# Kernel optimization log

Hardware: AMD Instinct MI355X
Metric: run time of the kernel (lower is better)

Reference implementation:

```python
import jax, jax.numpy as jnp
import numpy as np

N_NODES = 50000
N_EDGES = 800000
N_GRAPHS = 64
IN_C = 256      # num_commodities
HID = 256       # hidden_units
HID2 = HID // 2
N_DCS = 64


def setup_inputs() -> dict:
    key = jax.random.key(0)
    ks = jax.random.split(key, 8)
    x = jax.random.normal(ks[0], (N_NODES, IN_C), dtype=jnp.float32)
    edge_index = jax.random.randint(ks[1], (2, N_EDGES), 0, N_NODES, dtype=jnp.int32)
    # sorted graph-membership ids; even partition guarantees no empty graph
    batch = ((jnp.arange(N_NODES) * N_GRAPHS) // N_NODES).astype(jnp.int32)
    s1 = 1.0 / np.sqrt(IN_C)
    s2 = 1.0 / np.sqrt(HID)
    s3 = 1.0 / np.sqrt(HID2)
    W1 = jax.random.normal(ks[2], (IN_C, HID), dtype=jnp.float32) * s1
    b1 = jnp.zeros((HID,), dtype=jnp.float32)
    W2 = jax.random.normal(ks[3], (HID, HID2), dtype=jnp.float32) * s2
    b2 = jnp.zeros((HID2,), dtype=jnp.float32)
    Wm = jax.random.normal(ks[4], (HID2, N_DCS), dtype=jnp.float32) * s3
    bm = jax.random.normal(ks[5], (N_DCS,), dtype=jnp.float32) * s3
    return {"x": x, "edge_index": edge_index, "batch": batch,
            "W1": W1, "b1": b1, "W2": W2, "b2": b2, "Wm": Wm, "bm": bm}


def gcn_conv(x, W, b, src, dst, n_nodes):
    """PyG GCNConv: D^{-1/2}(A+I)D^{-1/2} X W + b (self-loops added)."""
    h = x @ W                                    # [N, out]
    ones = jnp.ones(src.shape[0], dtype=h.dtype)
    deg = jax.ops.segment_sum(ones, dst, num_segments=n_nodes) + 1.0  # +1 self-loop
    dis = jax.lax.rsqrt(deg)                     # deg >= 1, safe
    norm = dis[src] * dis[dst]                   # [E]
    agg = jax.ops.segment_sum(h[src] * norm[:, None], dst, num_segments=n_nodes)
    agg = agg + h * (dis * dis)[:, None]         # self-loop contribution
    return agg + b


def reference(x, edge_index, batch, W1, b1, W2, b2, Wm, bm):
    src, dst = edge_index[0], edge_index[1]
    n = x.shape[0]
    bx = jax.nn.relu(gcn_conv(x, W1, b1, src, dst, n))
    cx = jax.nn.relu(gcn_conv(bx, W2, b2, src, dst, n))
    px = jax.ops.segment_max(cx, batch, num_segments=N_GRAPHS)  # global max pool
    return px @ Wm + bm                           # [N_GRAPHS, N_DCS]
```

## Files before the change

### kernel.cpp

```cpp
#include <hip/hip_runtime.h>
#include <cstdint>


typedef _Float16 half2v __attribute__((ext_vector_type(2)));
typedef _Float16 half4v __attribute__((ext_vector_type(4)));
typedef _Float16 half8v __attribute__((ext_vector_type(8)));
typedef float f32x4 __attribute__((ext_vector_type(4)));

__device__ __forceinline__ void gl_lds16(const void* g, void* l) {
  __builtin_amdgcn_global_load_lds(
      (const __attribute__((address_space(1))) unsigned int*)g,
      (__attribute__((address_space(3))) unsigned int*)l, 16, 0, 0);
}

__global__ void deg_cvtw_k(const int* __restrict__ dst, int* __restrict__ deg,
                           int E, int ndeg,
                           const float* __restrict__ W1, _Float16* __restrict__ Wt1,
                           const float* __restrict__ W2, _Float16* __restrict__ Wt2) {
  const int b = blockIdx.x;
  if (b >= ndeg) {
    int i = (b - ndeg) * 256 + threadIdx.x;
    if (i < 256 * 256) {
      int k = i >> 8, c = i & 255;
      Wt1[c * 256 + k] = (_Float16)W1[i];
    } else {
      int j = i - 256 * 256;
      if (j < 256 * 128) {
        int k = j >> 7, c = j & 127;
        Wt2[c * 256 + k] = (_Float16)W2[j];
      }
    }
    return;
  }
  int i = b * blockDim.x + threadIdx.x;
  int e0 = i * 4;
  if (e0 + 4 <= E) {
    int4 d = *(const int4*)(dst + e0);
    atomicAdd(&deg[d.x], 1);
    atomicAdd(&deg[d.y], 1);
    atomicAdd(&deg[d.z], 1);
    atomicAdd(&deg[d.w], 1);
  } else {
    for (int e = e0; e < E; ++e) atomicAdd(&deg[dst[e]], 1);
  }
}

__global__ __launch_bounds__(256) void prep_k(const int* __restrict__ deg,
                                              int* __restrict__ offs,
                                              float* __restrict__ dis, int n) {
  __shared__ int sd[256];
  const int b = blockIdx.x;
  int pre = 0;
  for (int j = threadIdx.x; j < b * 256; j += 256) pre += deg[j];
  sd[threadIdx.x] = pre;
  __syncthreads();
  for (int s = 128; s > 0; s >>= 1) {
    if (threadIdx.x < s) sd[threadIdx.x] += sd[threadIdx.x + s];
    __syncthreads();
  }
  const int boff = sd[0];
  __syncthreads();
  int i = b * 256 + threadIdx.x;
  int v = (i < n) ? deg[i] : 0;
  if (i < n) dis[i] = rsqrtf((float)v + 1.0f);
  sd[threadIdx.x] = v;
  __syncthreads();
  for (int d = 1; d < 256; d <<= 1) {
    int t = (threadIdx.x >= d) ? sd[threadIdx.x - d] : 0;
    __syncthreads();
    sd[threadIdx.x] += t;
    __syncthreads();
  }
  if (i < n) offs[i] = boff + sd[threadIdx.x] - v;
  if (i == n - 1) offs[n] = boff + sd[threadIdx.x];
}

__global__ __launch_bounds__(256) void fill_gemm1_k(
    const int* __restrict__ src, const int* __restrict__ dstv,
    const int* __restrict__ offs, int* __restrict__ deg,
    unsigned short* __restrict__ csr, int E, int nfill,
    const float* __restrict__ A, const _Float16* __restrict__ Bt,
    const float* __restrict__ dis, _Float16* __restrict__ C, int M) {
  constexpr int K = 256, N = 256, BM = 64, BK = 32;
  __shared__ _Float16 As[BM * BK];
  __shared__ _Float16 Bs[N * BK];

  if (blockIdx.x < nfill) {
    int i = blockIdx.x * blockDim.x + threadIdx.x;
    int e0 = i * 4;
    if (e0 + 4 <= E) {
      int4 d = *(const int4*)(dstv + e0);
      int4 s = *(const int4*)(src + e0);
      int p0 = atomicSub(&deg[d.x], 1) - 1;
      csr[offs[d.x] + p0] = (unsigned short)s.x;
      int p1 = atomicSub(&deg[d.y], 1) - 1;
      csr[offs[d.y] + p1] = (unsigned short)s.y;
      int p2 = atomicSub(&deg[d.z], 1) - 1;
      csr[offs[d.z] + p2] = (unsigned short)s.z;
      int p3 = atomicSub(&deg[d.w], 1) - 1;
      csr[offs[d.w] + p3] = (unsigned short)s.w;
    } else {
      for (int e = e0; e < E; ++e) {
        int d = dstv[e];
        int pos = atomicSub(&deg[d], 1) - 1;
        csr[offs[d] + pos] = (unsigned short)src[e];
      }
    }
    return;
  }

  const int tid = threadIdx.x, lane = tid & 63, wave = tid >> 6;
  const int row0 = (blockIdx.x - nfill) * BM;
  const int kbase = (lane >> 4) * 8;
  const int r16 = lane & 15;

  int arow = row0 + wave * 16 + r16;
  if (arow > M - 1) arow = M - 1;
  const float* aSrc = A + (size_t)arow * K + kbase;
  _Float16* aDst = As + wave * 512 + lane * 8;

  const _Float16* bSrc[4];
  _Float16* bDst[4];
#pragma unroll
  for (int hh = 0; hh < 4; ++hh) {
    int fl = hh * 4 + wave;
    bSrc[hh] = Bt + (size_t)(fl * 16 + r16) * K + kbase;
    bDst[hh] = Bs + fl * 512;
  }

  f32x4 acc[4][4] = {};
  for (int k0 = 0; k0 < K; k0 += BK) {
#pragma unroll
    for (int hh = 0; hh < 4; ++hh) gl_lds16(bSrc[hh] + k0, bDst[hh]);
    float4 a0 = *(const float4*)(aSrc + k0);
    float4 a1 = *(const float4*)(aSrc + k0 + 4);
    half8v ah = {(_Float16)a0.x, (_Float16)a0.y, (_Float16)a0.z, (_Float16)a0.w,
                 (_Float16)a1.x, (_Float16)a1.y, (_Float16)a1.z, (_Float16)a1.w};
    *(half8v*)aDst = ah;
    __syncthreads();

    half8v af[4], bf[4];
#pragma unroll
    for (int m = 0; m < 4; ++m)
      af[m] = *(const half8v*)(As + m * 512 + lane * 8);
#pragma unroll
    for (int nj = 0; nj < 4; ++nj)
      bf[nj] = *(const half8v*)(Bs + (wave * 4 + nj) * 512 + lane * 8);
#pragma unroll
    for (int m = 0; m < 4; ++m)
#pragma unroll
      for (int nj = 0; nj < 4; ++nj)
        acc[m][nj] = __builtin_amdgcn_mfma_f32_16x16x32_f16(af[m], bf[nj], acc[m][nj], 0, 0, 0);
    __syncthreads();
  }

#pragma unroll
  for (int m = 0; m < 4; ++m) {
    const int rbase = row0 + m * 16 + (lane >> 4) * 4;
    float dr[4];
#pragma unroll
    for (int r = 0; r < 4; ++r) dr[r] = (rbase + r < M) ? dis[rbase + r] : 0.f;
#pragma unroll
    for (int nj = 0; nj < 4; ++nj) {
      int col = wave * 64 + nj * 16 + r16;
#pragma unroll
      for (int r = 0; r < 4; ++r) {
        int row = rbase + r;
        if (row < M) C[(size_t)row * N + col] = (_Float16)(acc[m][nj][r] * dr[r]);
      }
    }
  }
}

#define GBM 128
#define GBN 128
#define GBK 32

__global__ __launch_bounds__(256) void gemm_f16(const _Float16* __restrict__ A,
                                                const _Float16* __restrict__ Bt,
                                                const float* __restrict__ dis,
                                                _Float16* __restrict__ C,
                                                int M, int N, int K) {
  __shared__ _Float16 As[GBM * GBK];
  __shared__ _Float16 Bs[GBN * GBK];
  const int tid = threadIdx.x;
  const int lane = tid & 63;
  const int wave = tid >> 6;
  const int wm = wave >> 1, wn = wave & 1;
  const int row0 = blockIdx.x * GBM;
  const int col0 = blockIdx.y * GBN;

  f32x4 acc[4][4] = {};

  const int kbase = (lane >> 4) * 8;
  const _Float16* aSrc[2];
  _Float16* aDst[2];
  const _Float16* bSrc[2];
  _Float16* bDst[2];
#pragma unroll
  for (int h = 0; h < 2; ++h) {
    int fl = h * 4 + wave;
    int row = h * 64 + wave * 16 + (lane & 15);
    int gr = row0 + row;
    if (gr > M - 1) gr = M - 1;
    aSrc[h] = A + (size_t)gr * K + kbase;
    aDst[h] = As + fl * 512;
    int gc = col0 + row;
    bSrc[h] = Bt + (size_t)gc * K + kbase;
    bDst[h] = Bs + fl * 512;
  }

  for (int k0 = 0; k0 < K; k0 += GBK) {
    gl_lds16(aSrc[0] + k0, aDst[0]);
    gl_lds16(aSrc[1] + k0, aDst[1]);
    gl_lds16(bSrc[0] + k0, bDst[0]);
    gl_lds16(bSrc[1] + k0, bDst[1]);
    __syncthreads();

    half8v af[4], bf[4];
#pragma unroll
    for (int m = 0; m < 4; ++m)
      af[m] = *(const half8v*)(As + (wm * 4 + m) * 512 + lane * 8);
#pragma unroll
    for (int nj = 0; nj < 4; ++nj)
      bf[nj] = *(const half8v*)(Bs + (wn * 4 + nj) * 512 + lane * 8);
#pragma unroll
    for (int m = 0; m < 4; ++m)
#pragma unroll
      for (int nj = 0; nj < 4; ++nj)
        acc[m][nj] = __builtin_amdgcn_mfma_f32_16x16x32_f16(af[m], bf[nj], acc[m][nj], 0, 0, 0);
    __syncthreads();
  }

#pragma unroll
  for (int m = 0; m < 4; ++m) {
    const int rbase = row0 + wm * 64 + m * 16 + (lane >> 4) * 4;
    float dr[4];
#pragma unroll
    for (int r = 0; r < 4; ++r) dr[r] = (rbase + r < M) ? dis[rbase + r] : 0.f;
#pragma unroll
    for (int nj = 0; nj < 4; ++nj) {
      int col = col0 + wn * 64 + nj * 16 + (lane & 15);
#pragma unroll
      for (int r = 0; r < 4; ++r) {
        int row = rbase + r;
        if (row < M) C[(size_t)row * N + col] = (_Float16)(acc[m][nj][r] * dr[r]);
      }
    }
  }
}

template <int C, bool POOL>
__global__ __launch_bounds__(256) void agg_k(const _Float16* __restrict__ h,
                                             const float* __restrict__ dis,
                                             const int* __restrict__ offs,
                                             const unsigned short* __restrict__ csr,
                                             const float* __restrict__ bias,
                                             const int* __restrict__ batch,
                                             void* __restrict__ outv, int n) {
  constexpr int LPR = C / 8;
  constexpr int EPW = 64 / LPR;
  constexpr int U = 8;
  constexpr int EBLK = EPW * U;
  const int tid = threadIdx.x;
  const int lane = tid & 63;
  const int wave = tid >> 6;
  const int slot = lane / LPR;
  const int ch0 = (lane % LPR) * 8;

  const int wid = blockIdx.x * 4 + wave;
  const bool valid = wid < n;
  const int node = valid ? wid : n - 1;

  const int beg = offs[node], end = offs[node + 1];
  float acc[8] = {};
  int jb = beg;
  for (; jb + EBLK <= end; jb += EBLK) {
    half2v ah0[4] = {}, ah1[4] = {};
#pragma unroll
    for (int u = 0; u < U; ++u) {
      int s = csr[jb + u * EPW + slot];
      half8v hv = *(const half8v*)(h + (size_t)s * C + ch0);
      const half2v* hp = (const half2v*)&hv;
      if (u < 4) {
#pragma unroll
        for (int p = 0; p < 4; ++p) ah0[p] += hp[p];
      } else {
#pragma unroll
        for (int p = 0; p < 4; ++p) ah1[p] += hp[p];
      }
    }
#pragma unroll
    for (int p = 0; p < 4; ++p) {
      acc[2 * p + 0] += (float)ah0[p][0] + (float)ah1[p][0];
      acc[2 * p + 1] += (float)ah0[p][1] + (float)ah1[p][1];
    }
  }
  if (jb < end) {
    half2v ah0[4] = {}, ah1[4] = {};
#pragma unroll
    for (int u = 0; u < U; ++u) {
      int e = jb + u * EPW + slot;
      bool ok = e < end;
      int s = csr[ok ? e : end - 1];
      half8v hv = *(const half8v*)(h + (size_t)s * C + ch0);
      if (!ok) hv = half8v{};
      const half2v* hp = (const half2v*)&hv;
      if (u < 4) {
#pragma unroll
        for (int p = 0; p < 4; ++p) ah0[p] += hp[p];
      } else {
#pragma unroll
        for (int p = 0; p < 4; ++p) ah1[p] += hp[p];
      }
    }
#pragma unroll
    for (int p = 0; p < 4; ++p) {
      acc[2 * p + 0] += (float)ah0[p][0] + (float)ah1[p][0];
      acc[2 * p + 1] += (float)ah0[p][1] + (float)ah1[p][1];
    }
  }

  if constexpr (EPW == 4) {
#pragma unroll
    for (int v = 0; v < 8; ++v) {
      acc[v] += __shfl_xor(acc[v], 16);
      acc[v] += __shfl_xor(acc[v], 32);
    }
  } else {
#pragma unroll
    for (int v = 0; v < 8; ++v) acc[v] += __shfl_xor(acc[v], 32);
  }

  const float di = dis[node];
  half8v sv = *(const half8v*)(h + (size_t)node * C + ch0);
  float4 blo = *(const float4*)(bias + ch0);
  float4 bhi = *(const float4*)(bias + ch0 + 4);
  const float bb[8] = {blo.x, blo.y, blo.z, blo.w, bhi.x, bhi.y, bhi.z, bhi.w};
  float res[8];
#pragma unroll
  for (int v = 0; v < 8; ++v)
    res[v] = fmaxf((acc[v] + (float)sv[v]) * di + bb[v], 0.f);

  if constexpr (!POOL) {
    if (valid && lane < LPR) {
      half8v r;
#pragma unroll
      for (int v = 0; v < 8; ++v) r[v] = (_Float16)res[v];
      *(half8v*)((_Float16*)outv + (size_t)node * C + ch0) = r;
    }
  } else {
    __shared__ float pres[4][C];
    __shared__ int pg[4];
    __shared__ int uni;
    const int g = valid ? batch[node] : -1 - wave;
    if (lane < LPR) {
      *(f32x4*)&pres[wave][ch0] = f32x4{res[0], res[1], res[2], res[3]};
      *(f32x4*)&pres[wave][ch0 + 4] = f32x4{res[4], res[5], res[6], res[7]};
    }
    if (lane == 0) pg[wave] = g;
    __syncthreads();
    if (tid == 0) uni = (pg[0] == pg[1] && pg[1] == pg[2] && pg[2] == pg[3] && pg[0] >= 0);
    __syncthreads();
    float* px = (float*)outv;
    if (uni) {
      if (tid < C) {
        float m = fmaxf(fmaxf(pres[0][tid], pres[1][tid]),
                        fmaxf(pres[2][tid], pres[3][tid]));
        atomicMax((int*)&px[(size_t)pg[0] * C + tid], __float_as_int(m));
      }
    } else {
#pragma unroll
      for (int wv = 0; wv < 4; ++wv) {
        int gg = pg[wv];
        if (gg >= 0 && tid < C)
          atomicMax((int*)&px[(size_t)gg * C + tid], __float_as_int(pres[wv][tid]));
      }
    }
  }
}

__global__ void final_mm_k(const float* __restrict__ px, const float* __restrict__ Wm,
                           const float* __restrict__ bm, float* __restrict__ out) {
  int g = blockIdx.x;
  int c = threadIdx.x;
  float acc = bm[c];
#pragma unroll 8
  for (int k = 0; k < 128; ++k)
    acc = fmaf(px[g * 128 + k], Wm[k * 64 + c], acc);
  out[g * 64 + c] = acc;
}

extern "C" void kernel_launch(void* const* d_in, const int* in_sizes, int n_in,
                              void* d_out, int out_size, void* d_ws, size_t ws_size,
                              hipStream_t stream) {
  const float* x     = (const float*)d_in[0];
  const int*   ei    = (const int*)d_in[1];
  const int*   batch = (const int*)d_in[2];
  const float* W1    = (const float*)d_in[3];
  const float* b1    = (const float*)d_in[4];
  const float* W2    = (const float*)d_in[5];
  const float* b2    = (const float*)d_in[6];
  const float* Wm    = (const float*)d_in[7];
  const float* bm    = (const float*)d_in[8];
  float* out = (float*)d_out;

  const int E = in_sizes[1] / 2;
  const int n = in_sizes[2];
  const int HID = 256, HID2 = 128, NG = 64;
  const int* src = ei;
  const int* dst = ei + E;

  char* w = (char*)d_ws;
  size_t off = 0;
  auto alloc = [&](size_t bytes) -> void* {
    void* p = w + off;
    off = (off + bytes + 255) & ~(size_t)255;
    return p;
  };
  const int nb = (n + 255) / 256;
  int*            deg    = (int*)alloc((size_t)n * 4);
  float*          px     = (float*)alloc((size_t)NG * HID2 * 4);
  size_t          zlen   = off;
  float*          dis    = (float*)alloc((size_t)n * 4);
  int*            offs   = (int*)alloc((size_t)(n + 1) * 4);
  unsigned short* csr    = (unsigned short*)alloc((size_t)E * 2);
  _Float16*       Wt1    = (_Float16*)alloc((size_t)HID * 256 * 2);
  _Float16*       Wt2    = (_Float16*)alloc((size_t)HID2 * HID * 2);
  _Float16*       bufA   = (_Float16*)alloc((size_t)n * HID * 2);
  _Float16*       bufB   = (_Float16*)alloc((size_t)n * HID * 2);
  _Float16* h1 = bufA;
  _Float16* bx = bufB;
  _Float16* h2 = bufA;

  hipMemsetAsync(deg, 0, zlen, stream);

  const int ndeg = (E / 4 + 255) / 256;
  const int ncvt = (256 * 256 + 256 * 128) / 256;
  deg_cvtw_k<<<ndeg + ncvt, 256, 0, stream>>>(dst, deg, E, ndeg, W1, Wt1, W2, Wt2);
  prep_k<<<nb, 256, 0, stream>>>(deg, offs, dis, n);

  const int nfill = (E / 4 + 255) / 256;
  const int ng1 = (n + 63) / 64;
  fill_gemm1_k<<<nfill + ng1, 256, 0, stream>>>(src, dst, offs, deg, csr, E, nfill,
                                                x, Wt1, dis, h1, n);

  agg_k<256, false><<<(n + 3) / 4, 256, 0, stream>>>(h1, dis, offs, csr, b1, nullptr, bx, n);

  dim3 g2((n + GBM - 1) / GBM, HID2 / GBN);
  gemm_f16<<<g2, 256, 0, stream>>>(bx, Wt2, dis, h2, n, HID2, HID);
  agg_k<128, true><<<(n + 3) / 4, 256, 0, stream>>>(h2, dis, offs, csr, b2, batch, px, n);

  final_mm_k<<<NG, 64, 0, stream>>>(px, Wm, bm, out);
}
```

Before: 358.8 us.

## Split fused CSR-fill/GEMM1 kernel, prefetch A rows and batch gather loads

Splits the fused CSR fill + first GEMM kernel into two separate launches. The GEMM now loads its whole fp32 A row slice into registers up front, unrolls the K loop and sets occupancy launch bounds. The aggregation kernel first issues all index loads, then all feature gathers, before accumulating, which raises memory-level parallelism. The cost is higher register pressure and the loss of the overlap between the fill and GEMM work that the fused launch provided.

```diff
diff --git a/kernel.cpp b/kernel.cpp
--- a/kernel.cpp
+++ b/kernel.cpp
@@ -75,50 +75,62 @@
   if (i == n - 1) offs[n] = boff + sd[threadIdx.x];
 }
 
-__global__ __launch_bounds__(256) void fill_gemm1_k(
-    const int* __restrict__ src, const int* __restrict__ dstv,
-    const int* __restrict__ offs, int* __restrict__ deg,
-    unsigned short* __restrict__ csr, int E, int nfill,
-    const float* __restrict__ A, const _Float16* __restrict__ Bt,
-    const float* __restrict__ dis, _Float16* __restrict__ C, int M) {
+__global__ void fill_csr_k(const int* __restrict__ src, const int* __restrict__ dst,
+                           const int* __restrict__ offs, int* __restrict__ deg,
+                           unsigned short* __restrict__ csr, int E) {
+  int i = blockIdx.x * blockDim.x + threadIdx.x;
+  int e0 = i * 4;
+  if (e0 + 4 <= E) {
+    int4 d = *(const int4*)(dst + e0);
+    int4 s = *(const int4*)(src + e0);
+    int p0 = atomicSub(&deg[d.x], 1) - 1;
+    csr[offs[d.x] + p0] = (unsigned short)s.x;
+    int p1 = atomicSub(&deg[d.y], 1) - 1;
+    csr[offs[d.y] + p1] = (unsigned short)s.y;
+    int p2 = atomicSub(&deg[d.z], 1) - 1;
+    csr[offs[d.z] + p2] = (unsigned short)s.z;
+    int p3 = atomicSub(&deg[d.w], 1) - 1;
+    csr[offs[d.w] + p3] = (unsigned short)s.w;
+  } else {
+    for (int e = e0; e < E; ++e) {
+      int d = dst[e];
+      int pos = atomicSub(&deg[d], 1) - 1;
+      csr[offs[d] + pos] = (unsigned short)src[e];
+    }
+  }
+}
+
+__global__ __launch_bounds__(256, 4) void gemm1_k(const float* __restrict__ A,
+                                                  const _Float16* __restrict__ Bt,
+                                                  const float* __restrict__ dis,
+                                                  _Float16* __restrict__ C, int M) {
   constexpr int K = 256, N = 256, BM = 64, BK = 32;
   __shared__ _Float16 As[BM * BK];
   __shared__ _Float16 Bs[N * BK];
-
-  if (blockIdx.x < nfill) {
-    int i = blockIdx.x * blockDim.x + threadIdx.x;
-    int e0 = i * 4;
-    if (e0 + 4 <= E) {
-      int4 d = *(const int4*)(dstv + e0);
-      int4 s = *(const int4*)(src + e0);
-      int p0 = atomicSub(&deg[d.x], 1) - 1;
-      csr[offs[d.x] + p0] = (unsigned short)s.x;
-      int p1 = atomicSub(&deg[d.y], 1) - 1;
-      csr[offs[d.y] + p1] = (unsigned short)s.y;
-      int p2 = atomicSub(&deg[d.z], 1) - 1;
-      csr[offs[d.z] + p2] = (unsigned short)s.z;
-      int p3 = atomicSub(&deg[d.w], 1) - 1;
-      csr[offs[d.w] + p3] = (unsigned short)s.w;
-    } else {
-      for (int e = e0; e < E; ++e) {
-        int d = dstv[e];
-        int pos = atomicSub(&deg[d], 1) - 1;
-        csr[offs[d] + pos] = (unsigned short)src[e];
-      }
-    }
-    return;
-  }
-
   const int tid = threadIdx.x, lane = tid & 63, wave = tid >> 6;
-  const int row0 = (blockIdx.x - nfill) * BM;
+  const int row0 = blockIdx.x * BM;
   const int kbase = (lane >> 4) * 8;
   const int r16 = lane & 15;
 
   int arow = row0 + wave * 16 + r16;
   if (arow > M - 1) arow = M - 1;
   const float* aSrc = A + (size_t)arow * K + kbase;
+
+  float4 a0[8], a1[8];
+#pragma unroll
+  for (int i = 0; i < 8; ++i) {
+    a0[i] = *(const float4*)(aSrc + i * 32);
+    a1[i] = *(const float4*)(aSrc + i * 32 + 4);
+  }
+  half8v ah[8];
+#pragma unroll
+  for (int i = 0; i < 8; ++i) {
+    ah[i] = half8v{(_Float16)a0[i].x, (_Float16)a0[i].y, (_Float16)a0[i].z,
+                   (_Float16)a0[i].w, (_Float16)a1[i].x, (_Float16)a1[i].y,
+                   (_Float16)a1[i].z, (_Float16)a1[i].w};
+  }
+
   _Float16* aDst = As + wave * 512 + lane * 8;
-
   const _Float16* bSrc[4];
   _Float16* bDst[4];
 #pragma unroll
@@ -129,14 +141,12 @@
   }
 
   f32x4 acc[4][4] = {};
-  for (int k0 = 0; k0 < K; k0 += BK) {
+#pragma unroll
+  for (int it = 0; it < 8; ++it) {
+    const int k0 = it * BK;
 #pragma unroll
     for (int hh = 0; hh < 4; ++hh) gl_lds16(bSrc[hh] + k0, bDst[hh]);
-    float4 a0 = *(const float4*)(aSrc + k0);
-    float4 a1 = *(const float4*)(aSrc + k0 + 4);
-    half8v ah = {(_Float16)a0.x, (_Float16)a0.y, (_Float16)a0.z, (_Float16)a0.w,
-                 (_Float16)a1.x, (_Float16)a1.y, (_Float16)a1.z, (_Float16)a1.w};
-    *(half8v*)aDst = ah;
+    *(half8v*)aDst = ah[it];
     __syncthreads();
 
     half8v af[4], bf[4];
@@ -251,13 +261,13 @@
 }
 
 template <int C, bool POOL>
-__global__ __launch_bounds__(256) void agg_k(const _Float16* __restrict__ h,
-                                             const float* __restrict__ dis,
-                                             const int* __restrict__ offs,
-                                             const unsigned short* __restrict__ csr,
-                                             const float* __restrict__ bias,
-                                             const int* __restrict__ batch,
-                                             void* __restrict__ outv, int n) {
+__global__ __launch_bounds__(256, 6) void agg_k(const _Float16* __restrict__ h,
+                                                const float* __restrict__ dis,
+                                                const int* __restrict__ offs,
+                                                const unsigned short* __restrict__ csr,
+                                                const float* __restrict__ bias,
+                                                const int* __restrict__ batch,
+                                                void* __restrict__ outv, int n) {
   constexpr int LPR = C / 8;
   constexpr int EPW = 64 / LPR;
   constexpr int U = 8;
@@ -276,12 +286,17 @@
   float acc[8] = {};
   int jb = beg;
   for (; jb + EBLK <= end; jb += EBLK) {
+    int sidx[U];
+#pragma unroll
+    for (int u = 0; u < U; ++u) sidx[u] = csr[jb + u * EPW + slot];
+    half8v hv[U];
+#pragma unroll
+    for (int u = 0; u < U; ++u)
+      hv[u] = *(const half8v*)(h + (size_t)sidx[u] * C + ch0);
     half2v ah0[4] = {}, ah1[4] = {};
 #pragma unroll
     for (int u = 0; u < U; ++u) {
-      int s = csr[jb + u * EPW + slot];
-      half8v hv = *(const half8v*)(h + (size_t)s * C + ch0);
-      const half2v* hp = (const half2v*)&hv;
+      const half2v* hp = (const half2v*)&hv[u];
       if (u < 4) {
 #pragma unroll
         for (int p = 0; p < 4; ++p) ah0[p] += hp[p];
@@ -297,15 +312,23 @@
     }
   }
   if (jb < end) {
-    half2v ah0[4] = {}, ah1[4] = {};
+    int sidx[U];
+    bool ok[U];
 #pragma unroll
     for (int u = 0; u < U; ++u) {
       int e = jb + u * EPW + slot;
-      bool ok = e < end;
-      int s = csr[ok ? e : end - 1];
-      half8v hv = *(const half8v*)(h + (size_t)s * C + ch0);
-      if (!ok) hv = half8v{};
-      const half2v* hp = (const half2v*)&hv;
+      ok[u] = e < end;
+      sidx[u] = csr[ok[u] ? e : end - 1];
+    }
+    half8v hv[U];
+#pragma unroll
+    for (int u = 0; u < U; ++u)
+      hv[u] = *(const half8v*)(h + (size_t)sidx[u] * C + ch0);
+    half2v ah0[4] = {}, ah1[4] = {};
+#pragma unroll
+    for (int u = 0; u < U; ++u) {
+      if (!ok[u]) hv[u] = half8v{};
+      const half2v* hp = (const half2v*)&hv[u];
       if (u < 4) {
 #pragma unroll
         for (int p = 0; p < 4; ++p) ah0[p] += hp[p];
@@ -439,12 +462,9 @@
   const int ncvt = (256 * 256 + 256 * 128) / 256;
   deg_cvtw_k<<<ndeg + ncvt, 256, 0, stream>>>(dst, deg, E, ndeg, W1, Wt1, W2, Wt2);
   prep_k<<<nb, 256, 0, stream>>>(deg, offs, dis, n);
-
-  const int nfill = (E / 4 + 255) / 256;
-  const int ng1 = (n + 63) / 64;
-  fill_gemm1_k<<<nfill + ng1, 256, 0, stream>>>(src, dst, offs, deg, csr, E, nfill,
-                                                x, Wt1, dis, h1, n);
-
+  fill_csr_k<<<(E / 4 + 255) / 256, 256, 0, stream>>>(src, dst, offs, deg, csr, E);
+
+  gemm1_k<<<(n + 63) / 64, 256, 0, stream>>>(x, Wt1, dis, h1, n);
   agg_k<256, false><<<(n + 3) / 4, 256, 0, stream>>>(h1, dis, offs, csr, b1, nullptr, bx, n);
 
   dim3 g2((n + GBM - 1) / GBM, HID2 / GBN);
```

Measured after the change: 370.4 us. 1.03x slower.
